# Performance work log

Hardware: AMD Instinct MI355X
Metric: run time of the kernel (lower is better)

## Reference

```python
import jax, jax.numpy as jnp
import numpy as np

# ---- module hyperparameters (init_kwargs) ----
V0 = 1.0
SIGMA0 = 0.5
GAUSS_CONST = V0 / (np.sqrt(2.0 * np.pi) * SIGMA0)
NW, NF, D, H = 4096, 16, 3, 256  # walkers, fermions, dimensions, hidden width
N = NF * D


def setup_inputs() -> dict:
    key = jax.random.key(0)
    k0, k1, k2, k3 = jax.random.split(key, 4)
    sc = lambda k, shape, fan_in: jax.random.normal(k, shape, jnp.float32) / np.sqrt(fan_in).astype(np.float32)
    return {
        "x": jax.random.normal(k0, (NW, NF, D), jnp.float32),
        "W1": sc(k1, (N, H), N),
        "b1": jnp.zeros((H,), jnp.float32),
        "W2": sc(k2, (H, H), H),
        "b2": jnp.zeros((H,), jnp.float32),
        "w3": sc(k3, (H,), H),
        "b3": jnp.zeros((), jnp.float32),
    }


def _logpsi(xf, W1, b1, W2, b2, w3, b3):
    # xf: (N,) flattened single-walker coordinates -> scalar log|psi|
    h = jnp.tanh(xf @ W1 + b1)
    h = jnp.tanh(h @ W2 + b2)
    return h @ w3 + b3


def reference(x, W1, b1, W2, b2, w3, b3):
    nw, nf, d = x.shape
    xflat = x.reshape(nw, nf * d)

    f = lambda xf: _logpsi(xf, W1, b1, W2, b2, w3, b3)
    grad_f = jax.grad(f)

    def kinetic_one(xf):
        g = grad_f(xf)                      # (N,) d logpsi / dx
        hess = jax.jacfwd(grad_f)(xf)       # (N, N) forward-over-reverse Hessian
        lap = jnp.trace(hess)
        return -0.5 * (lap + jnp.sum(g * g))

    kin = jax.vmap(kinetic_one)(xflat)      # (nw,)

    # harmonic potential 1/2 sum x^2
    pot = 0.5 * jnp.sum(xflat * xflat, axis=1)

    # Gaussian interaction, faithful to source: unsqueeze(-2)/unsqueeze(-1) on
    # (nw, nf, d) broadcasts to (nw, nf, d, d) intra-particle coordinate diffs,
    # then sum over last axis -> (nw, nf, d), triu(k=1) over trailing (nf, d).
    diff = x[..., None, :] - x[..., :, None]            # (nw, nf, d, d)
    sqdist = jnp.sum(diff * diff, axis=-1)              # (nw, nf, d)
    mask = jnp.triu(jnp.ones((nf, d), x.dtype), k=1)    # (nf, d)
    inter = GAUSS_CONST * jnp.sum(jnp.exp(-sqdist / (2.0 * SIGMA0 ** 2)) * mask, axis=(-2, -1))

    eloc = kin + pot + inter
    return (eloc, kin, pot, inter)
```

## Files before the change

kernel.cpp:

```cpp
#include <hip/hip_runtime.h>
#include <cmath>

#define NWALK 4096
#define NXD   48
#define HID   256
#define WPB   8
#define GCONST 0.7978845608028654f

typedef _Float16 half8   __attribute__((ext_vector_type(8)));
typedef float    float4v __attribute__((ext_vector_type(4)));

__global__ __launch_bounds__(256) void prep_all(const float* __restrict__ W2,
                                                const float* __restrict__ W1,
                                                const float* __restrict__ x,
                                                const float* __restrict__ b1,
                                                _Float16* __restrict__ W2c,
                                                _Float16* __restrict__ W1c,
                                                _Float16* __restrict__ t1h,
                                                _Float16* __restrict__ h1h,
                                                _Float16* __restrict__ ch) {
    __shared__ float tile[64][65];
    __shared__ float xs[16][NXD];

    if (blockIdx.x < 16) {
        const int bi = blockIdx.x & 3;
        const int bj = blockIdx.x >> 2;
        const int tx = threadIdx.x & 63;
        const int ty = threadIdx.x >> 6;
        #pragma unroll
        for (int r = 0; r < 16; ++r) {
            int il = ty * 16 + r;
            tile[tx][il] = W2[(bi * 64 + il) * HID + bj * 64 + tx];
        }
        __syncthreads();
        #pragma unroll
        for (int r = 0; r < 16; ++r) {
            int jl = ty * 16 + r;
            W2c[(bj * 64 + jl) * HID + bi * 64 + tx] = (_Float16)tile[jl][tx];
        }
        #pragma unroll
        for (int r = 0; r < 3; ++r) {
            int k = blockIdx.x * 3 + r;
            W1c[k * HID + threadIdx.x] = (_Float16)W1[k * HID + threadIdx.x];
        }
    } else {
        const int i  = threadIdx.x;
        const int w0 = (blockIdx.x - 16) * 16;

        float col[NXD];
        float S = 0.f;
        #pragma unroll
        for (int k = 0; k < NXD; ++k) {
            float v = W1[k * HID + i];
            col[k] = v;
            S = fmaf(v, v, S);
        }
        #pragma unroll
        for (int t = threadIdx.x; t < 16 * NXD; t += 256)
            ((float*)xs)[t] = x[w0 * NXD + t];
        __syncthreads();

        const float b = b1[i];
        #pragma unroll 4
        for (int w = 0; w < 16; ++w) {
            float a1 = b;
            #pragma unroll
            for (int k = 0; k < NXD; ++k)
                a1 = fmaf(xs[w][k], col[k], a1);
            float h1 = tanhf(a1);
            float t1 = 1.f - h1 * h1;
            int off = (w0 + w) * HID + i;
            t1h[off] = (_Float16)t1;
            h1h[off] = (_Float16)h1;
            ch[off]  = (_Float16)(S * h1 * t1);
        }
    }
}

__global__ __launch_bounds__(256, 2) void eloc8(
    const float* __restrict__ x,
    const float* __restrict__ b2,
    const float* __restrict__ w3,
    const _Float16* __restrict__ W2c,
    const _Float16* __restrict__ W1c,
    const _Float16* __restrict__ t1h,
    const _Float16* __restrict__ h1h,
    const _Float16* __restrict__ ch,
    float* __restrict__ out)
{
    __shared__ __align__(16) _Float16 AsT[2][50 * HID];
    __shared__ float xs[WPB][NXD];
    __shared__ float b2s[HID], w3s[HID];
    __shared__ float a2s[HID], ps[HID], us[HID], uh2s[HID];
    __shared__ float gw[2][4][NXD];
    __shared__ float wred[2][4][2];

    const int w0   = blockIdx.x * WPB;
    const int tid  = threadIdx.x;
    const int wave = tid >> 6;
    const int lane = tid & 63;
    const int n16  = lane & 15;
    const int quad = (tid >> 4) & 3;
    const int ci   = tid & 31;
    const int k0   = tid >> 5;

    half8 afr[8][4];
    #pragma unroll
    for (int s = 0; s < 8; ++s)
        #pragma unroll
        for (int a = 0; a < 4; ++a)
            afr[s][a] = *(const half8*)(W2c + ((wave * 4 + a) * 16 + n16) * HID
                                        + s * 32 + quad * 8);

    b2s[tid] = b2[tid];
    w3s[tid] = w3[tid];
    #pragma unroll
    for (int t = tid; t < WPB * NXD; t += 256)
        ((float*)xs)[t] = x[w0 * NXD + t];

    {
        half8 th = *(const half8*)(t1h + w0 * HID + ci * 8);
        #pragma unroll
        for (int s2 = 0; s2 < 6; ++s2) {
            int k = s2 * 8 + k0;
            half8 wv = *(const half8*)(W1c + k * HID + ci * 8);
            *(half8*)(AsT[0] + k * HID + ((ci ^ (k & 7)) * 8)) = wv * th;
        }
        if (tid < 32) {
            half8 hv = *(const half8*)(h1h + w0 * HID + tid * 8);
            *(half8*)(AsT[0] + 48 * HID + tid * 8) = hv;
        } else if (tid < 64) {
            int c2 = tid - 32;
            half8 cv = *(const half8*)(ch + w0 * HID + c2 * 8);
            *(half8*)(AsT[0] + 49 * HID + ((c2 ^ 1) * 8)) = cv;
        }
    }
    __syncthreads();

    for (int ww = 0; ww < WPB; ++ww) {
        const int cur = ww & 1, nxt = cur ^ 1;
        const int wg  = w0 + ww;
        const _Float16* curA = AsT[cur];
        const bool more = (ww + 1 < WPB);

        {
            float4v acc[4];
            #pragma unroll
            for (int a = 0; a < 4; ++a) acc[a] = (float4v){0.f, 0.f, 0.f, 0.f};
            const int krow = 48 + (n16 & 1);
            #pragma unroll
            for (int s = 0; s < 8; ++s) {
                half8 bf = *(const half8*)(curA + krow * HID
                            + ((((s * 4 + quad) ^ (krow & 7)) << 3)));
                #pragma unroll
                for (int a = 0; a < 4; ++a)
                    acc[a] = __builtin_amdgcn_mfma_f32_16x16x32_f16(
                        afr[s][a], bf, acc[a], 0, 0, 0);
            }
            if (n16 == 0) {
                #pragma unroll
                for (int a = 0; a < 4; ++a)
                    #pragma unroll
                    for (int reg = 0; reg < 4; ++reg)
                        a2s[(wave * 4 + a) * 16 + quad * 4 + reg] = acc[a][reg];
            } else if (n16 == 1) {
                #pragma unroll
                for (int a = 0; a < 4; ++a)
                    #pragma unroll
                    for (int reg = 0; reg < 4; ++reg)
                        ps[(wave * 4 + a) * 16 + quad * 4 + reg] = acc[a][reg];
            }
        }

        float a2v = a2s[tid] + b2s[tid];
        float h2  = tanhf(a2v);
        float t2  = 1.f - h2 * h2;
        float u   = w3s[tid] * t2;
        us[tid]   = u;
        uh2s[tid] = u * h2;
        float rt2 = u * ps[tid];

        float uu_r[4][4], uh_r[4][4];
        #pragma unroll
        for (int a = 0; a < 4; ++a)
            #pragma unroll
            for (int reg = 0; reg < 4; ++reg) {
                int j = (wave * 4 + a) * 16 + quad * 4 + reg;
                uu_r[a][reg] = us[j];
                uh_r[a][reg] = uh2s[j];
            }

        float rt1 = 0.f;
        float gp[3];
        #pragma unroll 1
        for (int kt = 0; kt < 3; ++kt) {
            float4v acc[4];
            #pragma unroll
            for (int a = 0; a < 4; ++a) acc[a] = (float4v){0.f, 0.f, 0.f, 0.f};
            const int krow = kt * 16 + n16;
            #pragma unroll
            for (int s = 0; s < 8; ++s) {
                half8 bf = *(const half8*)(curA + krow * HID
                            + ((((s * 4 + quad) ^ (krow & 7)) << 3)));
                #pragma unroll
                for (int a = 0; a < 4; ++a)
                    acc[a] = __builtin_amdgcn_mfma_f32_16x16x32_f16(
                        afr[s][a], bf, acc[a], 0, 0, 0);
            }
            float g = 0.f;
            #pragma unroll
            for (int a = 0; a < 4; ++a)
                #pragma unroll
                for (int reg = 0; reg < 4; ++reg) {
                    float m = acc[a][reg];
                    rt1 = fmaf(m * m, uh_r[a][reg], rt1);
                    g   = fmaf(m, uu_r[a][reg], g);
                }
            gp[kt] = g;
        }

        if (more) {
            const int wn = wg + 1;
            half8 th = *(const half8*)(t1h + wn * HID + ci * 8);
            #pragma unroll
            for (int s2 = 0; s2 < 6; ++s2) {
                int k = s2 * 8 + k0;
                half8 wv = *(const half8*)(W1c + k * HID + ci * 8);
                *(half8*)(AsT[nxt] + k * HID + ((ci ^ (k & 7)) * 8)) = wv * th;
            }
            if (tid < 32) {
                half8 hv = *(const half8*)(h1h + wn * HID + tid * 8);
                *(half8*)(AsT[nxt] + 48 * HID + tid * 8) = hv;
            } else if (tid < 64) {
                half8 cv = *(const half8*)(ch + wn * HID + (tid - 32) * 8);
                *(half8*)(AsT[nxt] + 49 * HID + (((tid - 32) ^ 1) * 8)) = cv;
            }
        }

        #pragma unroll
        for (int off = 32; off > 0; off >>= 1) {
            rt1 += __shfl_down(rt1, off, 64);
            rt2 += __shfl_down(rt2, off, 64);
        }
        #pragma unroll
        for (int kt = 0; kt < 3; ++kt) {
            gp[kt] += __shfl_xor(gp[kt], 16, 64);
            gp[kt] += __shfl_xor(gp[kt], 32, 64);
        }
        if (lane == 0) { wred[cur][wave][0] = rt1; wred[cur][wave][1] = rt2; }
        if (lane < 16) {
            #pragma unroll
            for (int kt = 0; kt < 3; ++kt) gw[cur][wave][kt * 16 + lane] = gp[kt];
        }

        __syncthreads();

        if (wave == 0) {
            float ggp = 0.f, potp = 0.f;
            if (lane < NXD) {
                float g = gw[cur][0][lane] + gw[cur][1][lane]
                        + gw[cur][2][lane] + gw[cur][3][lane];
                ggp = g * g;
                float xq = xs[ww][lane];
                potp = 0.5f * xq * xq;
            }
            #pragma unroll
            for (int off = 32; off > 0; off >>= 1) {
                ggp  += __shfl_down(ggp, off, 64);
                potp += __shfl_down(potp, off, 64);
            }
            if (lane == 0) {
                float T1 = wred[cur][0][0] + wred[cur][1][0] + wred[cur][2][0] + wred[cur][3][0];
                float T2 = wred[cur][0][1] + wred[cur][1][1] + wred[cur][2][1] + wred[cur][3][1];
                float kin = T1 + T2 - 0.5f * ggp;

                float x0 = xs[ww][0], x1 = xs[ww][1], x2 = xs[ww][2];
                float x3 = xs[ww][3], x4 = xs[ww][4], x5 = xs[ww][5];
                float d01 = (x0-x1)*(x0-x1) + (x2-x1)*(x2-x1);
                float d02 = (x0-x2)*(x0-x2) + (x1-x2)*(x1-x2);
                float d12 = (x3-x5)*(x3-x5) + (x4-x5)*(x4-x5);
                float inter = GCONST * (expf(-2.f*d01) + expf(-2.f*d02) + expf(-2.f*d12));

                out[wg]             = kin + potp + inter;
                out[NWALK + wg]     = kin;
                out[2 * NWALK + wg] = potp;
                out[3 * NWALK + wg] = inter;
            }
        }
    }
}

extern "C" void kernel_launch(void* const* d_in, const int* in_sizes, int n_in,
                              void* d_out, int out_size, void* d_ws, size_t ws_size,
                              hipStream_t stream) {
    const float* x  = (const float*)d_in[0];
    const float* W1 = (const float*)d_in[1];
    const float* b1 = (const float*)d_in[2];
    const float* W2 = (const float*)d_in[3];
    const float* b2 = (const float*)d_in[4];
    const float* w3 = (const float*)d_in[5];
    float* out = (float*)d_out;

    char* ws = (char*)d_ws;
    _Float16* W2c = (_Float16*)(ws);
    _Float16* W1c = (_Float16*)(ws + 131072);
    _Float16* t1h = (_Float16*)(ws + 155648);
    _Float16* h1h = (_Float16*)(ws + 2252800);
    _Float16* chv = (_Float16*)(ws + 4349952);

    prep_all<<<16 + NWALK / 16, 256, 0, stream>>>(W2, W1, x, b1, W2c, W1c, t1h, h1h, chv);
    eloc8<<<NWALK / WPB, 256, 0, stream>>>(x, b2, w3, W2c, W1c, t1h, h1h, chv, out);
}
```

Before: 121.1 us.

## Split second-layer forward pass into separate prep2 kernel and defer per-walker reductions

Moves the per-walker second-layer MFMA (h1 and ch rows), tanh, and the u/uh/rt2 computation into a new prep2 kernel that batches 8 walkers per MFMA tile and writes u, u*h2 and rt2 to global workspace. The main kernel then only runs the 48-row Hessian MFMAs per walker and reads u/uh from global memory. W1 fragments are cached in registers, MFMA sections get raised priority, and the final reductions and output writes are deferred until after the walker loop instead of running serially per walker. This removes a dependent MFMA-then-tanh stage and an extra shared round trip from each iteration, at the cost of an extra kernel launch and several MB of added global traffic.

```diff
diff --git a/kernel.cpp b/kernel.cpp
--- a/kernel.cpp
+++ b/kernel.cpp
@@ -77,23 +77,102 @@
     }
 }
 
+__global__ __launch_bounds__(256) void prep2(
+    const float* __restrict__ b2, const float* __restrict__ w3,
+    const _Float16* __restrict__ W2c,
+    const _Float16* __restrict__ h1h, const _Float16* __restrict__ ch,
+    float* __restrict__ uf, float* __restrict__ uhf, float* __restrict__ rt2g)
+{
+    __shared__ float b2s[HID], w3s[HID];
+    __shared__ float r2s[4][8];
+
+    const int tid  = threadIdx.x;
+    const int wave = tid >> 6;
+    const int lane = tid & 63;
+    const int n16  = lane & 15;
+    const int quad = lane >> 4;
+    const int w0   = blockIdx.x * 8;
+
+    b2s[tid] = b2[tid];
+    w3s[tid] = w3[tid];
+
+    half8 afr[8][4];
+    #pragma unroll
+    for (int s = 0; s < 8; ++s)
+        #pragma unroll
+        for (int a = 0; a < 4; ++a)
+            afr[s][a] = *(const half8*)(W2c + ((wave * 4 + a) * 16 + n16) * HID
+                                        + s * 32 + quad * 8);
+
+    const _Float16* src  = (n16 & 1) ? ch : h1h;
+    const _Float16* brow = src + (size_t)(w0 + (n16 >> 1)) * HID;
+
+    float4v acc[4];
+    #pragma unroll
+    for (int a = 0; a < 4; ++a) acc[a] = (float4v){0.f, 0.f, 0.f, 0.f};
+    #pragma unroll
+    for (int s = 0; s < 8; ++s) {
+        half8 bf = *(const half8*)(brow + (s * 4 + quad) * 8);
+        #pragma unroll
+        for (int a = 0; a < 4; ++a)
+            acc[a] = __builtin_amdgcn_mfma_f32_16x16x32_f16(afr[s][a], bf, acc[a], 0, 0, 0);
+    }
+
+    __syncthreads();
+
+    const int w = n16 >> 1;
+    float um[4][4];
+    #pragma unroll
+    for (int a = 0; a < 4; ++a)
+        #pragma unroll
+        for (int reg = 0; reg < 4; ++reg) um[a][reg] = 0.f;
+
+    if (!(n16 & 1)) {
+        #pragma unroll
+        for (int a = 0; a < 4; ++a)
+            #pragma unroll
+            for (int reg = 0; reg < 4; ++reg) {
+                int i   = (wave * 4 + a) * 16 + quad * 4 + reg;
+                float a2 = acc[a][reg] + b2s[i];
+                float h2 = tanhf(a2);
+                float t2 = 1.f - h2 * h2;
+                float u  = w3s[i] * t2;
+                um[a][reg] = u;
+                uf [(size_t)(w0 + w) * HID + i] = u;
+                uhf[(size_t)(w0 + w) * HID + i] = u * h2;
+            }
+    }
+
+    float part = 0.f;
+    #pragma unroll
+    for (int a = 0; a < 4; ++a)
+        #pragma unroll
+        for (int reg = 0; reg < 4; ++reg) {
+            float uo = __shfl_xor(um[a][reg], 1, 64);
+            part = fmaf(uo, acc[a][reg], part);
+        }
+    part += __shfl_xor(part, 16, 64);
+    part += __shfl_xor(part, 32, 64);
+    if (quad == 0 && (n16 & 1)) r2s[wave][w] = part;
+    __syncthreads();
+    if (tid < 8)
+        rt2g[w0 + tid] = r2s[0][tid] + r2s[1][tid] + r2s[2][tid] + r2s[3][tid];
+}
+
 __global__ __launch_bounds__(256, 2) void eloc8(
     const float* __restrict__ x,
-    const float* __restrict__ b2,
-    const float* __restrict__ w3,
     const _Float16* __restrict__ W2c,
     const _Float16* __restrict__ W1c,
     const _Float16* __restrict__ t1h,
-    const _Float16* __restrict__ h1h,
-    const _Float16* __restrict__ ch,
+    const float* __restrict__ uf,
+    const float* __restrict__ uhf,
+    const float* __restrict__ rt2g,
     float* __restrict__ out)
 {
-    __shared__ __align__(16) _Float16 AsT[2][50 * HID];
+    __shared__ __align__(16) _Float16 AsT[2][48 * HID];
     __shared__ float xs[WPB][NXD];
-    __shared__ float b2s[HID], w3s[HID];
-    __shared__ float a2s[HID], ps[HID], us[HID], uh2s[HID];
-    __shared__ float gw[2][4][NXD];
-    __shared__ float wred[2][4][2];
+    __shared__ float gw[WPB][4][NXD];
+    __shared__ float rt1p[WPB][4][16];
 
     const int w0   = blockIdx.x * WPB;
     const int tid  = threadIdx.x;
@@ -112,42 +191,51 @@
             afr[s][a] = *(const half8*)(W2c + ((wave * 4 + a) * 16 + n16) * HID
                                         + s * 32 + quad * 8);
 
-    b2s[tid] = b2[tid];
-    w3s[tid] = w3[tid];
+    half8 w1r[6];
+    #pragma unroll
+    for (int s2 = 0; s2 < 6; ++s2)
+        w1r[s2] = *(const half8*)(W1c + (s2 * 8 + k0) * HID + ci * 8);
+
     #pragma unroll
     for (int t = tid; t < WPB * NXD; t += 256)
         ((float*)xs)[t] = x[w0 * NXD + t];
 
     {
-        half8 th = *(const half8*)(t1h + w0 * HID + ci * 8);
+        half8 th = *(const half8*)(t1h + (size_t)w0 * HID + ci * 8);
         #pragma unroll
         for (int s2 = 0; s2 < 6; ++s2) {
             int k = s2 * 8 + k0;
-            half8 wv = *(const half8*)(W1c + k * HID + ci * 8);
-            *(half8*)(AsT[0] + k * HID + ((ci ^ (k & 7)) * 8)) = wv * th;
-        }
-        if (tid < 32) {
-            half8 hv = *(const half8*)(h1h + w0 * HID + tid * 8);
-            *(half8*)(AsT[0] + 48 * HID + tid * 8) = hv;
-        } else if (tid < 64) {
-            int c2 = tid - 32;
-            half8 cv = *(const half8*)(ch + w0 * HID + c2 * 8);
-            *(half8*)(AsT[0] + 49 * HID + ((c2 ^ 1) * 8)) = cv;
+            *(half8*)(AsT[0] + k * HID + ((ci ^ (k & 7)) * 8)) = w1r[s2] * th;
         }
     }
     __syncthreads();
 
+    #pragma unroll 1
     for (int ww = 0; ww < WPB; ++ww) {
         const int cur = ww & 1, nxt = cur ^ 1;
         const int wg  = w0 + ww;
         const _Float16* curA = AsT[cur];
         const bool more = (ww + 1 < WPB);
 
-        {
+        const int wn = more ? (wg + 1) : wg;
+        half8 th = *(const half8*)(t1h + (size_t)wn * HID + ci * 8);
+
+        const float* ub = uf  + (size_t)wg * HID + wave * 64 + quad * 4;
+        const float* hb = uhf + (size_t)wg * HID + wave * 64 + quad * 4;
+        float4v uu[4], uh[4];
+        #pragma unroll
+        for (int a = 0; a < 4; ++a) uu[a] = *(const float4v*)(ub + a * 16);
+        #pragma unroll
+        for (int a = 0; a < 4; ++a) uh[a] = *(const float4v*)(hb + a * 16);
+
+        float rt1 = 0.f;
+        #pragma unroll 1
+        for (int kt = 0; kt < 3; ++kt) {
             float4v acc[4];
             #pragma unroll
             for (int a = 0; a < 4; ++a) acc[a] = (float4v){0.f, 0.f, 0.f, 0.f};
-            const int krow = 48 + (n16 & 1);
+            const int krow = kt * 16 + n16;
+            __builtin_amdgcn_s_setprio(1);
             #pragma unroll
             for (int s = 0; s < 8; ++s) {
                 half8 bf = *(const half8*)(curA + krow * HID
@@ -157,136 +245,87 @@
                     acc[a] = __builtin_amdgcn_mfma_f32_16x16x32_f16(
                         afr[s][a], bf, acc[a], 0, 0, 0);
             }
-            if (n16 == 0) {
-                #pragma unroll
-                for (int a = 0; a < 4; ++a)
-                    #pragma unroll
-                    for (int reg = 0; reg < 4; ++reg)
-                        a2s[(wave * 4 + a) * 16 + quad * 4 + reg] = acc[a][reg];
-            } else if (n16 == 1) {
-                #pragma unroll
-                for (int a = 0; a < 4; ++a)
-                    #pragma unroll
-                    for (int reg = 0; reg < 4; ++reg)
-                        ps[(wave * 4 + a) * 16 + quad * 4 + reg] = acc[a][reg];
-            }
-        }
-
-        float a2v = a2s[tid] + b2s[tid];
-        float h2  = tanhf(a2v);
-        float t2  = 1.f - h2 * h2;
-        float u   = w3s[tid] * t2;
-        us[tid]   = u;
-        uh2s[tid] = u * h2;
-        float rt2 = u * ps[tid];
-
-        float uu_r[4][4], uh_r[4][4];
-        #pragma unroll
-        for (int a = 0; a < 4; ++a)
-            #pragma unroll
-            for (int reg = 0; reg < 4; ++reg) {
-                int j = (wave * 4 + a) * 16 + quad * 4 + reg;
-                uu_r[a][reg] = us[j];
-                uh_r[a][reg] = uh2s[j];
-            }
-
-        float rt1 = 0.f;
-        float gp[3];
-        #pragma unroll 1
-        for (int kt = 0; kt < 3; ++kt) {
-            float4v acc[4];
-            #pragma unroll
-            for (int a = 0; a < 4; ++a) acc[a] = (float4v){0.f, 0.f, 0.f, 0.f};
-            const int krow = kt * 16 + n16;
-            #pragma unroll
-            for (int s = 0; s < 8; ++s) {
-                half8 bf = *(const half8*)(curA + krow * HID
-                            + ((((s * 4 + quad) ^ (krow & 7)) << 3)));
-                #pragma unroll
-                for (int a = 0; a < 4; ++a)
-                    acc[a] = __builtin_amdgcn_mfma_f32_16x16x32_f16(
-                        afr[s][a], bf, acc[a], 0, 0, 0);
-            }
+            __builtin_amdgcn_s_setprio(0);
             float g = 0.f;
             #pragma unroll
             for (int a = 0; a < 4; ++a)
                 #pragma unroll
                 for (int reg = 0; reg < 4; ++reg) {
                     float m = acc[a][reg];
-                    rt1 = fmaf(m * m, uh_r[a][reg], rt1);
-                    g   = fmaf(m, uu_r[a][reg], g);
+                    rt1 = fmaf(m * m, uh[a][reg], rt1);
+                    g   = fmaf(m, uu[a][reg], g);
                 }
-            gp[kt] = g;
-        }
+            g += __shfl_xor(g, 16, 64);
+            g += __shfl_xor(g, 32, 64);
+            if (lane < 16) gw[ww][wave][kt * 16 + lane] = g;
+        }
+
+        rt1 += __shfl_xor(rt1, 16, 64);
+        rt1 += __shfl_xor(rt1, 32, 64);
+        if (lane < 16) rt1p[ww][wave][lane] = rt1;
 
         if (more) {
-            const int wn = wg + 1;
-            half8 th = *(const half8*)(t1h + wn * HID + ci * 8);
             #pragma unroll
             for (int s2 = 0; s2 < 6; ++s2) {
                 int k = s2 * 8 + k0;
-                half8 wv = *(const half8*)(W1c + k * HID + ci * 8);
-                *(half8*)(AsT[nxt] + k * HID + ((ci ^ (k & 7)) * 8)) = wv * th;
+                *(half8*)(AsT[nxt] + k * HID + ((ci ^ (k & 7)) * 8)) = w1r[s2] * th;
             }
-            if (tid < 32) {
-                half8 hv = *(const half8*)(h1h + wn * HID + tid * 8);
-                *(half8*)(AsT[nxt] + 48 * HID + tid * 8) = hv;
-            } else if (tid < 64) {
-                half8 cv = *(const half8*)(ch + wn * HID + (tid - 32) * 8);
-                *(half8*)(AsT[nxt] + 49 * HID + (((tid - 32) ^ 1) * 8)) = cv;
-            }
-        }
-
-        #pragma unroll
-        for (int off = 32; off > 0; off >>= 1) {
-            rt1 += __shfl_down(rt1, off, 64);
-            rt2 += __shfl_down(rt2, off, 64);
-        }
-        #pragma unroll
-        for (int kt = 0; kt < 3; ++kt) {
-            gp[kt] += __shfl_xor(gp[kt], 16, 64);
-            gp[kt] += __shfl_xor(gp[kt], 32, 64);
-        }
-        if (lane == 0) { wred[cur][wave][0] = rt1; wred[cur][wave][1] = rt2; }
-        if (lane < 16) {
-            #pragma unroll
-            for (int kt = 0; kt < 3; ++kt) gw[cur][wave][kt * 16 + lane] = gp[kt];
-        }
-
+        }
         __syncthreads();
-
-        if (wave == 0) {
-            float ggp = 0.f, potp = 0.f;
-            if (lane < NXD) {
-                float g = gw[cur][0][lane] + gw[cur][1][lane]
-                        + gw[cur][2][lane] + gw[cur][3][lane];
-                ggp = g * g;
-                float xq = xs[ww][lane];
-                potp = 0.5f * xq * xq;
-            }
-            #pragma unroll
-            for (int off = 32; off > 0; off >>= 1) {
-                ggp  += __shfl_down(ggp, off, 64);
-                potp += __shfl_down(potp, off, 64);
-            }
-            if (lane == 0) {
-                float T1 = wred[cur][0][0] + wred[cur][1][0] + wred[cur][2][0] + wred[cur][3][0];
-                float T2 = wred[cur][0][1] + wred[cur][1][1] + wred[cur][2][1] + wred[cur][3][1];
-                float kin = T1 + T2 - 0.5f * ggp;
-
-                float x0 = xs[ww][0], x1 = xs[ww][1], x2 = xs[ww][2];
-                float x3 = xs[ww][3], x4 = xs[ww][4], x5 = xs[ww][5];
-                float d01 = (x0-x1)*(x0-x1) + (x2-x1)*(x2-x1);
-                float d02 = (x0-x2)*(x0-x2) + (x1-x2)*(x1-x2);
-                float d12 = (x3-x5)*(x3-x5) + (x4-x5)*(x4-x5);
-                float inter = GCONST * (expf(-2.f*d01) + expf(-2.f*d02) + expf(-2.f*d12));
-
-                out[wg]             = kin + potp + inter;
-                out[NWALK + wg]     = kin;
-                out[2 * NWALK + wg] = potp;
-                out[3 * NWALK + wg] = inter;
-            }
-        }
+    }
+
+    const int wa = 2 * wave, wb = wa + 1;
+    float rt2a = rt2g[w0 + wa];
+    float rt2b = rt2g[w0 + wb];
+
+    float r0 = rt1p[wa][quad][n16];
+    float r1 = rt1p[wb][quad][n16];
+
+    float ga = 0.f, gb = 0.f, xa = 0.f, xb = 0.f;
+    if (lane < NXD) {
+        ga = gw[wa][0][lane] + gw[wa][1][lane] + gw[wa][2][lane] + gw[wa][3][lane];
+        gb = gw[wb][0][lane] + gw[wb][1][lane] + gw[wb][2][lane] + gw[wb][3][lane];
+        xa = xs[wa][lane];
+        xb = xs[wb][lane];
+    }
+    float gga = ga * ga, ggb = gb * gb;
+    float pa = 0.5f * xa * xa, pb = 0.5f * xb * xb;
+    #pragma unroll
+    for (int off = 32; off > 0; off >>= 1) {
+        r0  += __shfl_down(r0,  off, 64);
+        r1  += __shfl_down(r1,  off, 64);
+        gga += __shfl_down(gga, off, 64);
+        ggb += __shfl_down(ggb, off, 64);
+        pa  += __shfl_down(pa,  off, 64);
+        pb  += __shfl_down(pb,  off, 64);
+    }
+    if (lane == 0) {
+        float kina = r0 + rt2a - 0.5f * gga;
+        float kinb = r1 + rt2b - 0.5f * ggb;
+
+        float x0 = xs[wa][0], x1 = xs[wa][1], x2 = xs[wa][2];
+        float x3 = xs[wa][3], x4 = xs[wa][4], x5 = xs[wa][5];
+        float d01 = (x0-x1)*(x0-x1) + (x2-x1)*(x2-x1);
+        float d02 = (x0-x2)*(x0-x2) + (x1-x2)*(x1-x2);
+        float d12 = (x3-x5)*(x3-x5) + (x4-x5)*(x4-x5);
+        float intera = GCONST * (expf(-2.f*d01) + expf(-2.f*d02) + expf(-2.f*d12));
+
+        x0 = xs[wb][0]; x1 = xs[wb][1]; x2 = xs[wb][2];
+        x3 = xs[wb][3]; x4 = xs[wb][4]; x5 = xs[wb][5];
+        float e01 = (x0-x1)*(x0-x1) + (x2-x1)*(x2-x1);
+        float e02 = (x0-x2)*(x0-x2) + (x1-x2)*(x1-x2);
+        float e12 = (x3-x5)*(x3-x5) + (x4-x5)*(x4-x5);
+        float interb = GCONST * (expf(-2.f*e01) + expf(-2.f*e02) + expf(-2.f*e12));
+
+        const int wga = w0 + wa, wgb = w0 + wb;
+        out[wga]             = kina + pa + intera;
+        out[NWALK + wga]     = kina;
+        out[2 * NWALK + wga] = pa;
+        out[3 * NWALK + wga] = intera;
+        out[wgb]             = kinb + pb + interb;
+        out[NWALK + wgb]     = kinb;
+        out[2 * NWALK + wgb] = pb;
+        out[3 * NWALK + wgb] = interb;
     }
 }
 
@@ -307,7 +346,11 @@
     _Float16* t1h = (_Float16*)(ws + 155648);
     _Float16* h1h = (_Float16*)(ws + 2252800);
     _Float16* chv = (_Float16*)(ws + 4349952);
+    float*    uf  = (float*)(ws + 6447104);
+    float*    uhf = (float*)(ws + 10641408);
+    float*    r2g = (float*)(ws + 14835712);
 
     prep_all<<<16 + NWALK / 16, 256, 0, stream>>>(W2, W1, x, b1, W2c, W1c, t1h, h1h, chv);
-    eloc8<<<NWALK / WPB, 256, 0, stream>>>(x, b2, w3, W2c, W1c, t1h, h1h, chv, out);
+    prep2<<<NWALK / 8, 256, 0, stream>>>(b2, w3, W2c, h1h, chv, uf, uhf, r2g);
+    eloc8<<<NWALK / WPB, 256, 0, stream>>>(x, W2c, W1c, t1h, uf, uhf, r2g, out);
 }
```

After: 123.2 us. About the same (+1.7%).
